# Kernel optimization log

Hardware: AMD Instinct MI355X
Metric: run time of the kernel (lower is better)

Reference implementation:

```python
import jax, jax.numpy as jnp
import numpy as np

KSIZE = 5
# OpenCV: sigma=0 -> sigma = 0.3*((ksize-1)*0.5 - 1) + 0.8
SIGMA = 0.3 * ((KSIZE - 1) * 0.5 - 1.0) + 0.8  # = 1.1 for ksize=5


def _gauss_taps(ksize, sigma):
    r = (ksize - 1) / 2.0
    xs = np.arange(ksize, dtype=np.float64) - r
    w = np.exp(-(xs ** 2) / (2.0 * sigma ** 2))
    w /= w.sum()
    return jnp.asarray(w, dtype=jnp.float32)


def setup_inputs() -> dict:
    key = jax.random.key(0)
    x = jax.random.normal(key, (64, 384, 512, 3), dtype=jnp.float32)
    return {"x": x}


def reference(x):
    # Separable 5x5 Gaussian blur, OpenCV default border BORDER_REFLECT_101
    # (numpy/jnp 'reflect' mode, edge pixel not repeated).
    w = _gauss_taps(KSIZE, SIGMA)  # [5]
    pad = KSIZE // 2
    B, H, W, C = x.shape
    # vertical pass
    xp = jnp.pad(x, ((0, 0), (pad, pad), (0, 0), (0, 0)), mode="reflect")
    y = sum(w[k] * xp[:, k:k + H, :, :] for k in range(KSIZE))
    # horizontal pass
    yp = jnp.pad(y, ((0, 0), (0, 0), (pad, pad), (0, 0)), mode="reflect")
    out = sum(w[k] * yp[:, :, k:k + W, :] for k in range(KSIZE))
    return out
```

## Files before the change

kernel.cpp:

```cpp
#include <hip/hip_runtime.h>


#define BN 64
#define HN 384
#define WN 512
#define CN 3
#define ROWF (WN * CN)
#define ROWQ (ROWF / 4)
#define TH 8
#define NTILES (HN / TH)
#define NTHREADS 256
#define ITERS ((TH * ROWQ) / NTHREADS)

#define CW0 0.07076630f
#define CW1 0.24446040f
#define CW2 0.36954650f

__global__ __launch_bounds__(NTHREADS) void gauss_blur_fused(
        const float* __restrict__ x, float* __restrict__ out) {
    __shared__ float v[TH * ROWF];

    const int tile = blockIdx.x;
    const int b    = tile / NTILES;
    const int h0   = (tile - b * NTILES) * TH;
    const float* __restrict__ xb = x + (size_t)b * HN * ROWF;
    float* __restrict__ ob = out + (size_t)b * HN * ROWF + (size_t)h0 * ROWF;

    for (int i = 0; i < ITERS; ++i) {
        int idx = threadIdx.x + i * NTHREADS;
        int r = idx / ROWQ;
        int q = idx - r * ROWQ;
        int h = h0 + r;
        float4 acc = make_float4(0.f, 0.f, 0.f, 0.f);
#pragma unroll
        for (int k = 0; k < 5; ++k) {
            int hs = h + k - 2;
            hs = hs < 0 ? -hs : hs;
            hs = hs >= HN ? 2 * HN - 2 - hs : hs;
            float wk = (k == 2) ? CW2 : ((k == 1 || k == 3) ? CW1 : CW0);
            const float4 t = ((const float4*)(xb + (size_t)hs * ROWF))[q];
            acc.x += wk * t.x;
            acc.y += wk * t.y;
            acc.z += wk * t.z;
            acc.w += wk * t.w;
        }
        ((float4*)v)[idx] = acc;
    }
    __syncthreads();

    for (int i = 0; i < ITERS; ++i) {
        int idx = threadIdx.x + i * NTHREADS;
        int r = idx / ROWQ;
        int q = idx - r * ROWQ;
        const float* vr = v + r * ROWF;
        float4 res;
        if (q >= 2 && q < ROWQ - 2) {
            float wnd[20];
#pragma unroll
            for (int j = 0; j < 5; ++j) {
                float4 t = ((const float4*)vr)[q - 2 + j];
                wnd[4 * j + 0] = t.x;
                wnd[4 * j + 1] = t.y;
                wnd[4 * j + 2] = t.z;
                wnd[4 * j + 3] = t.w;
            }
#pragma unroll
            for (int j = 0; j < 4; ++j) {
                ((float*)&res)[j] =
                    CW0 * (wnd[j + 2] + wnd[j + 14]) +
                    CW1 * (wnd[j + 5] + wnd[j + 11]) +
                    CW2 * wnd[j + 8];
            }
        } else {
#pragma unroll
            for (int j = 0; j < 4; ++j) {
                int e  = 4 * q + j;
                int wp = e / 3;
                int c  = e - wp * 3;
                float s = 0.f;
#pragma unroll
                for (int k = 0; k < 5; ++k) {
                    int ws = wp + k - 2;
                    ws = ws < 0 ? -ws : ws;
                    ws = ws >= WN ? 2 * WN - 2 - ws : ws;
                    float wk = (k == 2) ? CW2 : ((k == 1 || k == 3) ? CW1 : CW0);
                    s += wk * vr[ws * 3 + c];
                }
                ((float*)&res)[j] = s;
            }
        }
        ((float4*)ob)[idx] = res;
    }
}

extern "C" void kernel_launch(void* const* d_in, const int* in_sizes, int n_in,
                              void* d_out, int out_size, void* d_ws, size_t ws_size,
                              hipStream_t stream) {
    const float* x = (const float*)d_in[0];
    float* out = (float*)d_out;
    gauss_blur_fused<<<dim3(BN * NTILES), dim3(NTHREADS), 0, stream>>>(x, out);
}
```

Baseline: 274.0 us.

## Reuse vertical input rows in registers with one thread per column quad

```diff
diff --git a/kernel.cpp b/kernel.cpp
--- a/kernel.cpp
+++ b/kernel.cpp
@@ -7,16 +7,15 @@
 #define CN 3
 #define ROWF (WN * CN)
 #define ROWQ (ROWF / 4)
-#define TH 8
+#define TH 4
 #define NTILES (HN / TH)
-#define NTHREADS 256
-#define ITERS ((TH * ROWQ) / NTHREADS)
+#define NT 384
 
 #define CW0 0.07076630f
 #define CW1 0.24446040f
 #define CW2 0.36954650f
 
-__global__ __launch_bounds__(NTHREADS) void gauss_blur_fused(
+__global__ __launch_bounds__(NT, 8) void gauss_blur_fused(
         const float* __restrict__ x, float* __restrict__ out) {
     __shared__ float v[TH * ROWF];
 
@@ -26,35 +25,35 @@
     const float* __restrict__ xb = x + (size_t)b * HN * ROWF;
     float* __restrict__ ob = out + (size_t)b * HN * ROWF + (size_t)h0 * ROWF;
 
-    for (int i = 0; i < ITERS; ++i) {
-        int idx = threadIdx.x + i * NTHREADS;
-        int r = idx / ROWQ;
-        int q = idx - r * ROWQ;
-        int h = h0 + r;
-        float4 acc = make_float4(0.f, 0.f, 0.f, 0.f);
+    const int q = threadIdx.x;
+
+    float4 rowv[TH + 4];
 #pragma unroll
-        for (int k = 0; k < 5; ++k) {
-            int hs = h + k - 2;
-            hs = hs < 0 ? -hs : hs;
-            hs = hs >= HN ? 2 * HN - 2 - hs : hs;
-            float wk = (k == 2) ? CW2 : ((k == 1 || k == 3) ? CW1 : CW0);
-            const float4 t = ((const float4*)(xb + (size_t)hs * ROWF))[q];
-            acc.x += wk * t.x;
-            acc.y += wk * t.y;
-            acc.z += wk * t.z;
-            acc.w += wk * t.w;
-        }
-        ((float4*)v)[idx] = acc;
+    for (int i = 0; i < TH + 4; ++i) {
+        int hs = h0 + i - 2;
+        hs = hs < 0 ? -hs : hs;
+        hs = hs >= HN ? 2 * HN - 2 - hs : hs;
+        rowv[i] = ((const float4*)(xb + (size_t)hs * ROWF))[q];
+    }
+#pragma unroll
+    for (int r = 0; r < TH; ++r) {
+        float4 a;
+        a.x = CW0 * (rowv[r].x + rowv[r + 4].x) +
+              CW1 * (rowv[r + 1].x + rowv[r + 3].x) + CW2 * rowv[r + 2].x;
+        a.y = CW0 * (rowv[r].y + rowv[r + 4].y) +
+              CW1 * (rowv[r + 1].y + rowv[r + 3].y) + CW2 * rowv[r + 2].y;
+        a.z = CW0 * (rowv[r].z + rowv[r + 4].z) +
+              CW1 * (rowv[r + 1].z + rowv[r + 3].z) + CW2 * rowv[r + 2].z;
+        a.w = CW0 * (rowv[r].w + rowv[r + 4].w) +
+              CW1 * (rowv[r + 1].w + rowv[r + 3].w) + CW2 * rowv[r + 2].w;
+        ((float4*)v)[r * ROWQ + q] = a;
     }
     __syncthreads();
 
-    for (int i = 0; i < ITERS; ++i) {
-        int idx = threadIdx.x + i * NTHREADS;
-        int r = idx / ROWQ;
-        int q = idx - r * ROWQ;
-        const float* vr = v + r * ROWF;
-        float4 res;
-        if (q >= 2 && q < ROWQ - 2) {
+    if (q >= 2 && q < ROWQ - 2) {
+#pragma unroll
+        for (int r = 0; r < TH; ++r) {
+            const float* vr = v + r * ROWF;
             float wnd[20];
 #pragma unroll
             for (int j = 0; j < 5; ++j) {
@@ -64,6 +63,7 @@
                 wnd[4 * j + 2] = t.z;
                 wnd[4 * j + 3] = t.w;
             }
+            float4 res;
 #pragma unroll
             for (int j = 0; j < 4; ++j) {
                 ((float*)&res)[j] =
@@ -71,7 +71,13 @@
                     CW1 * (wnd[j + 5] + wnd[j + 11]) +
                     CW2 * wnd[j + 8];
             }
-        } else {
+            ((float4*)ob)[r * ROWQ + q] = res;
+        }
+    } else {
+#pragma unroll
+        for (int r = 0; r < TH; ++r) {
+            const float* vr = v + r * ROWF;
+            float4 res;
 #pragma unroll
             for (int j = 0; j < 4; ++j) {
                 int e  = 4 * q + j;
@@ -88,8 +94,8 @@
                 }
                 ((float*)&res)[j] = s;
             }
+            ((float4*)ob)[r * ROWQ + q] = res;
         }
-        ((float4*)ob)[idx] = res;
     }
 }
 
@@ -98,5 +104,5 @@
                               hipStream_t stream) {
     const float* x = (const float*)d_in[0];
     float* out = (float*)d_out;
-    gauss_blur_fused<<<dim3(BN * NTILES), dim3(NTHREADS), 0, stream>>>(x, out);
+    gauss_blur_fused<<<dim3(BN * NTILES), dim3(NT), 0, stream>>>(x, out);
 }
```

New measurement: 265.1 us. 3.2% less time.
